# Kernel optimization log

Hardware: AMD Instinct MI355X
Metric: run time of the kernel (lower is better)

The kernel has to match this reference:

```python
import jax, jax.numpy as jnp
import numpy as np

D, DK, DV, H, DFF = 1024, 64, 64, 16, 4096
B, LD, LE = 8, 1024, 1024
NEG = -1e9


def _ln(x, g, b, eps=1e-5):
    m = jnp.mean(x, axis=-1, keepdims=True)
    v = jnp.var(x, axis=-1, keepdims=True)
    return (x - m) / jnp.sqrt(v + eps) * g + b


def _mha(q_src, kv_src, wq, bq, wk, bk, wv, bv, mask):
    # wq/wk: [H, D, DK], wv: [H, D, DV]; per-head linear projections (with bias)
    Q = jnp.einsum('bld,hdk->bhlk', q_src, wq) + bq[:, None, :]
    K = jnp.einsum('bld,hdk->bhlk', kv_src, wk) + bk[:, None, :]
    V = jnp.einsum('bld,hdv->bhlv', kv_src, wv) + bv[:, None, :]
    s = jnp.einsum('bhqk,bhmk->bhqm', Q, K) / jnp.sqrt(jnp.asarray(DK, Q.dtype))
    if mask is not None:
        s = s + mask
    a = jax.nn.softmax(s, axis=-1)
    o = jnp.einsum('bhqm,bhmv->bhqv', a, V)  # [B,H,L,DV]
    b_, h_, l_, dv_ = o.shape
    return jnp.transpose(o, (0, 2, 1, 3)).reshape(b_, l_, h_ * dv_)


def setup_inputs() -> dict:
    key = jax.random.key(0)
    ks = jax.random.split(key, 24)
    sc = 0.02
    inp = {
        'decoder_embedding': jax.random.normal(ks[0], (B, LD, D), jnp.float32),
        'encoder_output': jax.random.normal(ks[1], (B, LE, D), jnp.float32),
        # masked (self) attention heads, stacked over H
        'm_wq': jax.random.normal(ks[2], (H, D, DK)) * sc,
        'm_bq': jnp.zeros((H, DK)),
        'm_wk': jax.random.normal(ks[3], (H, D, DK)) * sc,
        'm_bk': jnp.zeros((H, DK)),
        'm_wv': jax.random.normal(ks[4], (H, D, DV)) * sc,
        'm_bv': jnp.zeros((H, DV)),
        # cross attention heads
        'c_wq': jax.random.normal(ks[5], (H, D, DK)) * sc,
        'c_bq': jnp.zeros((H, DK)),
        'c_wk': jax.random.normal(ks[6], (H, D, DK)) * sc,
        'c_bk': jnp.zeros((H, DK)),
        'c_wv': jax.random.normal(ks[7], (H, D, DV)) * sc,
        'c_bv': jnp.zeros((H, DV)),
        # FFN
        'ff_w1': jax.random.normal(ks[8], (D, DFF)) * sc,
        'ff_b1': jnp.zeros((DFF,)),
        'ff_w2': jax.random.normal(ks[9], (DFF, D)) * sc,
        'ff_b2': jnp.zeros((D,)),
        # LayerNorms (ln2 reused for the third norm, as in the source)
        'ln1_g': jnp.ones((D,)), 'ln1_b': jnp.zeros((D,)),
        'ln2_g': jnp.ones((D,)), 'ln2_b': jnp.zeros((D,)),
    }
    return inp


def reference(decoder_embedding, encoder_output,
              m_wq, m_bq, m_wk, m_bk, m_wv, m_bv,
              c_wq, c_bq, c_wk, c_bk, c_wv, c_bv,
              ff_w1, ff_b1, ff_w2, ff_b2,
              ln1_g, ln1_b, ln2_g, ln2_b):
    Ld = decoder_embedding.shape[1]
    causal = jnp.where(jnp.tril(jnp.ones((Ld, Ld), bool)), 0.0, NEG)[None, None]
    # masked self-attention + residual + LN1
    sa = _mha(decoder_embedding, decoder_embedding, m_wq, m_bq, m_wk, m_bk, m_wv, m_bv, causal)
    x = _ln(decoder_embedding + sa, ln1_g, ln1_b)
    # cross-attention (Q from decoder, K/V from encoder) + residual + LN2
    ca = _mha(x, encoder_output, c_wq, c_bq, c_wk, c_bk, c_wv, c_bv, None)
    x = _ln(x + ca, ln2_g, ln2_b)
    # FFN + residual + LN2 again (source reuses layer_norm2)
    ff = jnp.maximum(x @ ff_w1 + ff_b1, 0.0) @ ff_w2 + ff_b2
    return _ln(x + ff, ln2_g, ln2_b)
```

## Files before the change

kernel.cpp:

```cpp
#include <hip/hip_runtime.h>
#include <hip/hip_bf16.h>
#include <cstdint>

typedef __bf16 bf16x8 __attribute__((ext_vector_type(8)));
typedef float f32x4 __attribute__((ext_vector_type(4)));

union U128 { uint4 u; __bf16 h[8]; };
union U64  { uint2 u; __bf16 h[4]; };

#define DMODEL 1024
#define NHEAD  16
#define DHEAD  64

__device__ __forceinline__ void async_copy16(const void* g, void* l) {
  __builtin_amdgcn_global_load_lds(
      (const __attribute__((address_space(1))) void*)g,
      (__attribute__((address_space(3))) void*)l, 16, 0, 0);
}

__global__ __launch_bounds__(256) void k_cast(const float* __restrict__ s,
    __bf16* __restrict__ d, int n) {
  int i = (blockIdx.x * 256 + threadIdx.x) * 4;
  if (i < n) {
    float4 v = *(const float4*)(s + i);
    U64 o;
    o.h[0] = (__bf16)v.x; o.h[1] = (__bf16)v.y;
    o.h[2] = (__bf16)v.z; o.h[3] = (__bf16)v.w;
    *(uint2*)(d + i) = o.u;
  }
}

__global__ __launch_bounds__(256) void k_pack(float* __restrict__ dst,
    const float* __restrict__ s0, const float* __restrict__ s1,
    const float* __restrict__ s2, int n) {
  int i = blockIdx.x * 256 + threadIdx.x;
  if (i < n) dst[i] = s0[i];
  else if (i < 2 * n) dst[i] = s1[i - n];
  else if (i < 3 * n) dst[i] = s2[i - 2 * n];
}

__global__ __launch_bounds__(256) void k_transpose(const float* __restrict__ src,
    __bf16* __restrict__ dst, int R, int C) {
  __shared__ __bf16 tile[32][33];
  src += (size_t)blockIdx.z * R * C;
  dst += (size_t)blockIdx.z * R * C;
  int c0 = blockIdx.x * 32, r0 = blockIdx.y * 32;
  int tx = threadIdx.x & 31, ty = threadIdx.x >> 5;
  for (int i = ty; i < 32; i += 8)
    tile[i][tx] = (__bf16)src[(size_t)(r0 + i) * C + (c0 + tx)];
  __syncthreads();
  for (int i = ty; i < 32; i += 8)
    dst[(size_t)(c0 + i) * R + (r0 + tx)] = tile[tx][i];
}

template<bool RELU, typename OutT>
__global__ __launch_bounds__(256, 3) void k_gemm(const __bf16* __restrict__ A,
    const __bf16* __restrict__ Bt, const float* __restrict__ bias,
    OutT* __restrict__ C, int M, int N, int K) {
  __shared__ __bf16 As[128][64];
  __shared__ __bf16 Bs[128][64];
  const int m0 = blockIdx.y * 128, n0 = blockIdx.x * 128;
  const int t = threadIdx.x;
  const int wave = t >> 6, lane = t & 63;
  const int wm = (wave & 1) * 64, wn = (wave >> 1) * 64;
  const int lrow = lane & 15, quad = lane >> 4;
  const int r8 = lane >> 3;
  const int gG = (lane & 7) ^ (r8 & 7);
  const __bf16* Ap[4]; const __bf16* Bp[4];
  __bf16* lA[4]; __bf16* lB[4];
  for (int j = 0; j < 4; j++) {
    int rr = wave * 8 + j * 32 + r8;
    Ap[j] = A  + (size_t)(m0 + rr) * K + gG * 8;
    Bp[j] = Bt + (size_t)(n0 + rr) * K + gG * 8;
    lA[j] = &As[wave * 8 + j * 32][0];
    lB[j] = &Bs[wave * 8 + j * 32][0];
  }
  f32x4 acc[4][4] = {};
  for (int k0 = 0; k0 < K; k0 += 64) {
    __syncthreads();
    for (int j = 0; j < 4; j++) {
      async_copy16(Ap[j] + k0, lA[j]);
      async_copy16(Bp[j] + k0, lB[j]);
    }
    __syncthreads();
    for (int ks = 0; ks < 2; ks++) {
      bf16x8 af[4], bfv[4];
      for (int i = 0; i < 4; i++) {
        int ra = wm + i * 16 + lrow, rb = wn + i * 16 + lrow;
        af[i]  = *(const bf16x8*)&As[ra][(((ks * 4 + quad) ^ (ra & 7))) * 8];
        bfv[i] = *(const bf16x8*)&Bs[rb][(((ks * 4 + quad) ^ (rb & 7))) * 8];
      }
      for (int mi = 0; mi < 4; mi++)
        for (int ni = 0; ni < 4; ni++)
          acc[mi][ni] = __builtin_amdgcn_mfma_f32_16x16x32_bf16(af[mi], bfv[ni], acc[mi][ni], 0, 0, 0);
    }
  }
  for (int ni = 0; ni < 4; ni++) {
    int col = n0 + wn + ni * 16 + lrow;
    float bv = bias[col];
    for (int mi = 0; mi < 4; mi++) {
      int row = m0 + wm + mi * 16 + quad * 4;
      for (int r = 0; r < 4; r++) {
        float v = acc[mi][ni][r] + bv;
        if (RELU) v = fmaxf(v, 0.f);
        C[(size_t)(row + r) * N + col] = (OutT)v;
      }
    }
  }
}

template<bool CAUSAL>
__global__ __launch_bounds__(256, 4) void k_attn(const __bf16* __restrict__ Q,
    const __bf16* __restrict__ Kg, const __bf16* __restrict__ Vg,
    float* __restrict__ O, int Lq, int Lk, int qs, int kvs) {
  __shared__ alignas(16) __bf16 Qs[64][72];
  __shared__ alignas(16) __bf16 Ks[64][72];
  __shared__ alignas(16) __bf16 Vt[64][72];
  __shared__ alignas(16) __bf16 Ps[64][72];
  const int t = threadIdx.x;
  const int wave = t >> 6, lane = t & 63;
  const int lrow = lane & 15, quad = lane >> 4;
  const int wm16 = wave * 16;
  const int qt = CAUSAL ? (gridDim.x - 1 - blockIdx.x) : blockIdx.x;
  const int q0 = qt * 64;
  const int b = blockIdx.y >> 4, h = blockIdx.y & 15;
  const __bf16* Qb = Q  + (size_t)b * Lq * qs  + h * DHEAD;
  const __bf16* Kb = Kg + (size_t)b * Lk * kvs + h * DHEAD;
  const __bf16* Vb = Vg + (size_t)b * Lk * kvs + h * DHEAD;
  {
    int row = t >> 3, col = (t & 7) * 8;
    U128 u0, u1;
    u0.u = *(const uint4*)(Qb + (size_t)(q0 + row) * qs + col);
    u1.u = *(const uint4*)(Qb + (size_t)(q0 + row + 32) * qs + col);
    for (int j = 0; j < 8; j++) {
      u0.h[j] = (__bf16)((float)u0.h[j] * 0.125f);
      u1.h[j] = (__bf16)((float)u1.h[j] * 0.125f);
    }
    *(uint4*)&Qs[row][col]      = u0.u;
    *(uint4*)&Qs[row + 32][col] = u1.u;
  }
  f32x4 acc_o[4] = {};
  float m_r[4] = {-1e30f, -1e30f, -1e30f, -1e30f};
  float l_r[4] = {};
  const int nkt = CAUSAL ? (qt + 1) : (Lk / 64);
  const int krow = t >> 3, kcol = (t & 7) * 8;
  const int vkk = t & 63, vd8 = t >> 6;
  for (int kt = 0; kt < nkt; kt++) {
    const int k0 = kt * 64;
    uint4 ka  = *(const uint4*)(Kb + (size_t)(k0 + krow) * kvs + kcol);
    uint4 ka2 = *(const uint4*)(Kb + (size_t)(k0 + krow + 32) * kvs + kcol);
    uint4 va  = *(const uint4*)(Vb + (size_t)(k0 + vkk) * kvs + vd8 * 8);
    uint4 va2 = *(const uint4*)(Vb + (size_t)(k0 + vkk) * kvs + (vd8 + 4) * 8);
    __syncthreads();
    *(uint4*)&Ks[krow][kcol]      = ka;
    *(uint4*)&Ks[krow + 32][kcol] = ka2;
    { U128 u; u.u = va;  for (int j = 0; j < 8; j++) Vt[vd8 * 8 + j][vkk] = u.h[j]; }
    { U128 u; u.u = va2; for (int j = 0; j < 8; j++) Vt[(vd8 + 4) * 8 + j][vkk] = u.h[j]; }
    __syncthreads();
    f32x4 accs[4] = {};
    for (int ks = 0; ks < 2; ks++) {
      bf16x8 qa = *(const bf16x8*)&Qs[wm16 + lrow][ks * 32 + quad * 8];
      for (int nb = 0; nb < 4; nb++) {
        bf16x8 kfr = *(const bf16x8*)&Ks[nb * 16 + lrow][ks * 32 + quad * 8];
        accs[nb] = __builtin_amdgcn_mfma_f32_16x16x32_bf16(qa, kfr, accs[nb], 0, 0, 0);
      }
    }
    float pm[4] = {-1e30f, -1e30f, -1e30f, -1e30f};
    for (int nb = 0; nb < 4; nb++)
      for (int r = 0; r < 4; r++) {
        float s = accs[nb][r];
        if (CAUSAL && kt == qt)
          s = ((nb * 16 + lrow) <= (wm16 + quad * 4 + r)) ? s : -1e30f;
        accs[nb][r] = s;
        pm[r] = fmaxf(pm[r], s);
      }
    for (int msk = 1; msk <= 8; msk <<= 1)
      for (int r = 0; r < 4; r++)
        pm[r] = fmaxf(pm[r], __shfl_xor(pm[r], msk));
    float alpha[4], rs[4];
    for (int r = 0; r < 4; r++) {
      float mn = fmaxf(m_r[r], pm[r]);
      alpha[r] = __expf(m_r[r] - mn);
      m_r[r] = mn;
      float srow = 0.f;
      for (int nb = 0; nb < 4; nb++) {
        float p = __expf(accs[nb][r] - mn);
        accs[nb][r] = p;
        srow += p;
      }
      rs[r] = srow;
    }
    for (int msk = 1; msk <= 8; msk <<= 1)
      for (int r = 0; r < 4; r++)
        rs[r] += __shfl_xor(rs[r], msk);
    for (int r = 0; r < 4; r++)
      l_r[r] = l_r[r] * alpha[r] + rs[r];
    for (int ni = 0; ni < 4; ni++)
      for (int r = 0; r < 4; r++)
        acc_o[ni][r] *= alpha[r];
    for (int nb = 0; nb < 4; nb++)
      for (int r = 0; r < 4; r++)
        Ps[wm16 + quad * 4 + r][nb * 16 + lrow] = (__bf16)accs[nb][r];
    for (int ks = 0; ks < 2; ks++) {
      bf16x8 pa = *(const bf16x8*)&Ps[wm16 + lrow][ks * 32 + quad * 8];
      for (int ni = 0; ni < 4; ni++) {
        bf16x8 vfr = *(const bf16x8*)&Vt[ni * 16 + lrow][ks * 32 + quad * 8];
        acc_o[ni] = __builtin_amdgcn_mfma_f32_16x16x32_bf16(pa, vfr, acc_o[ni], 0, 0, 0);
      }
    }
  }
  float* Ob = O + (size_t)b * Lq * DMODEL + h * DHEAD;
  for (int r = 0; r < 4; r++) {
    float linv = 1.f / fmaxf(l_r[r], 1e-30f);
    int q = wm16 + quad * 4 + r;
    for (int ni = 0; ni < 4; ni++)
      Ob[(size_t)(q0 + q) * DMODEL + ni * 16 + lrow] = acc_o[ni][r] * linv;
  }
}

template<typename ResT, typename OutT>
__global__ __launch_bounds__(256) void k_ln_add(const ResT* __restrict__ a,
    const float* __restrict__ bres, const float* __restrict__ g,
    const float* __restrict__ be, OutT* __restrict__ out) {
  __shared__ float red[2][4];
  const int r = blockIdx.x, t = threadIdx.x;
  const size_t base = (size_t)r * DMODEL + t * 4;
  float x[4];
  for (int i = 0; i < 4; i++) x[i] = (float)a[base + i] + bres[base + i];
  float s  = x[0] + x[1] + x[2] + x[3];
  float s2 = x[0]*x[0] + x[1]*x[1] + x[2]*x[2] + x[3]*x[3];
  for (int off = 32; off > 0; off >>= 1) {
    s  += __shfl_down(s, off);
    s2 += __shfl_down(s2, off);
  }
  if ((t & 63) == 0) { red[0][t >> 6] = s; red[1][t >> 6] = s2; }
  __syncthreads();
  s  = red[0][0] + red[0][1] + red[0][2] + red[0][3];
  s2 = red[1][0] + red[1][1] + red[1][2] + red[1][3];
  const float mean = s * (1.f / DMODEL);
  const float var  = s2 * (1.f / DMODEL) - mean * mean;
  const float rstd = rsqrtf(var + 1e-5f);
  for (int i = 0; i < 4; i++)
    out[base + i] = (OutT)((x[i] - mean) * rstd * g[t * 4 + i] + be[t * 4 + i]);
}

extern "C" void kernel_launch(void* const* d_in, const int* in_sizes, int n_in,
                              void* d_out, int out_size, void* d_ws, size_t ws_size,
                              hipStream_t stream) {
  (void)in_sizes; (void)n_in; (void)out_size; (void)ws_size;
  const float* dec   = (const float*)d_in[0];
  const float* enc   = (const float*)d_in[1];
  const float* m_wq  = (const float*)d_in[2];
  const float* m_bq  = (const float*)d_in[3];
  const float* m_wk  = (const float*)d_in[4];
  const float* m_bk  = (const float*)d_in[5];
  const float* m_wv  = (const float*)d_in[6];
  const float* m_bv  = (const float*)d_in[7];
  const float* c_wq  = (const float*)d_in[8];
  const float* c_bq  = (const float*)d_in[9];
  const float* c_wk  = (const float*)d_in[10];
  const float* c_bk  = (const float*)d_in[11];
  const float* c_wv  = (const float*)d_in[12];
  const float* c_bv  = (const float*)d_in[13];
  const float* ff_w1 = (const float*)d_in[14];
  const float* ff_b1 = (const float*)d_in[15];
  const float* ff_w2 = (const float*)d_in[16];
  const float* ff_b2 = (const float*)d_in[17];
  const float* ln1_g = (const float*)d_in[18];
  const float* ln1_b = (const float*)d_in[19];
  const float* ln2_g = (const float*)d_in[20];
  const float* ln2_b = (const float*)d_in[21];

  char* w = (char*)d_ws;
  __bf16* decB = (__bf16*)(w);
  __bf16* encB = (__bf16*)(w + (16ull << 20));
  __bf16* X1b  = decB;
  __bf16* X2b  = encB;
  __bf16* WB   = (__bf16*)(w + (32ull << 20));
  float*  BP   = (float*) (w + (38ull << 20));
  __bf16* QKV  = (__bf16*)(w + (40ull << 20));
  __bf16* KV   = (__bf16*)(w + (40ull << 20));
  __bf16* Qc   = (__bf16*)(w + (72ull << 20));
  __bf16* FF   = (__bf16*)(w + (40ull << 20));
  float*  AO   = (float*) (w + (104ull << 20));
  float* out = (float*)d_out;

  const int M = 8192, NTOK = M * DMODEL;
  dim3 blk(256);
  dim3 gC(NTOK / 1024);
  dim3 gT6(2, 32, 16);
  dim3 gA(16, 128);
  dim3 gL(M);

  k_cast<<<gC, blk, 0, stream>>>(dec, decB, NTOK);
  k_cast<<<gC, blk, 0, stream>>>(enc, encB, NTOK);

  k_transpose<<<gT6, blk, 0, stream>>>(m_wq, WB, 1024, 64);
  k_transpose<<<gT6, blk, 0, stream>>>(m_wk, WB + (1 << 20), 1024, 64);
  k_transpose<<<gT6, blk, 0, stream>>>(m_wv, WB + (2 << 20), 1024, 64);
  k_pack<<<dim3(12), blk, 0, stream>>>(BP, m_bq, m_bk, m_bv, 1024);
  k_gemm<false, __bf16><<<dim3(24, 64), blk, 0, stream>>>(decB, WB, BP, QKV, M, 3072, 1024);
  k_attn<true><<<gA, blk, 0, stream>>>(QKV, QKV + 1024, QKV + 2048, AO, 1024, 1024, 3072, 3072);
  k_ln_add<float, __bf16><<<gL, blk, 0, stream>>>(dec, AO, ln1_g, ln1_b, X1b);

  k_transpose<<<gT6, blk, 0, stream>>>(c_wk, WB, 1024, 64);
  k_transpose<<<gT6, blk, 0, stream>>>(c_wv, WB + (1 << 20), 1024, 64);
  k_transpose<<<gT6, blk, 0, stream>>>(c_wq, WB + (2 << 20), 1024, 64);
  k_pack<<<dim3(8), blk, 0, stream>>>(BP, c_bk, c_bv, c_bv, 1024);
  k_gemm<false, __bf16><<<dim3(16, 64), blk, 0, stream>>>(encB, WB, BP, KV, M, 2048, 1024);
  k_gemm<false, __bf16><<<dim3(8, 64), blk, 0, stream>>>(X1b, WB + (2 << 20), c_bq, Qc, M, 1024, 1024);
  k_attn<false><<<gA, blk, 0, stream>>>(Qc, KV, KV + 1024, AO, 1024, 1024, 1024, 2048);
  k_ln_add<__bf16, __bf16><<<gL, blk, 0, stream>>>(X1b, AO, ln2_g, ln2_b, X2b);

  k_transpose<<<dim3(128, 32, 1), blk, 0, stream>>>(ff_w1, WB, 1024, 4096);
  k_gemm<true, __bf16><<<dim3(32, 64), blk, 0, stream>>>(X2b, WB, ff_b1, FF, M, 4096, 1024);
  k_transpose<<<dim3(32, 128, 1), blk, 0, stream>>>(ff_w2, WB, 4096, 1024);
  k_gemm<false, float><<<dim3(8, 64), blk, 0, stream>>>(FF, WB, ff_b2, AO, M, 1024, 4096);
  k_ln_add<__bf16, float><<<gL, blk, 0, stream>>>(X2b, AO, ln2_g, ln2_b, out);
}
```

Baseline: 804.3 us.

## Restructure attention kernel: transposed S, register-resident P, double-buffered K/V

```diff
diff --git a/kernel.cpp b/kernel.cpp
--- a/kernel.cpp
+++ b/kernel.cpp
@@ -3,14 +3,53 @@
 #include <cstdint>
 
 typedef __bf16 bf16x8 __attribute__((ext_vector_type(8)));
+typedef __bf16 bf16x4 __attribute__((ext_vector_type(4)));
+typedef short  short4v __attribute__((ext_vector_type(4)));
+typedef _Float16 f16x4 __attribute__((ext_vector_type(4)));
 typedef float f32x4 __attribute__((ext_vector_type(4)));
 
 union U128 { uint4 u; __bf16 h[8]; };
 union U64  { uint2 u; __bf16 h[4]; };
+union PV4  { uint2 u; bf16x4 b; short4v s; f16x4 f; };
 
 #define DMODEL 1024
 #define NHEAD  16
 #define DHEAD  64
+
+#if __has_builtin(__builtin_amdgcn_mfma_f32_16x16x16_bf16)
+#define PV_F16 0
+__device__ __forceinline__ f32x4 mfma16(PV4 a, PV4 b, f32x4 c) {
+  return __builtin_amdgcn_mfma_f32_16x16x16_bf16(a.b, b.b, c, 0, 0, 0);
+}
+#elif __has_builtin(__builtin_amdgcn_mfma_f32_16x16x16bf16_1k)
+#define PV_F16 0
+__device__ __forceinline__ f32x4 mfma16(PV4 a, PV4 b, f32x4 c) {
+  return __builtin_amdgcn_mfma_f32_16x16x16bf16_1k(a.s, b.s, c, 0, 0, 0);
+}
+#else
+#define PV_F16 1
+__device__ __forceinline__ f32x4 mfma16(PV4 a, PV4 b, f32x4 c) {
+  return __builtin_amdgcn_mfma_f32_16x16x16f16(a.f, b.f, c, 0, 0, 0);
+}
+#endif
+
+__device__ __forceinline__ uint16_t pv_bits(__bf16 v) {
+#if PV_F16
+  union { _Float16 f; uint16_t u; } x; x.f = (_Float16)(float)v; return x.u;
+#else
+  union { __bf16 b; uint16_t u; } x; x.b = v; return x.u;
+#endif
+}
+
+__device__ __forceinline__ PV4 pack4(float a, float b, float c, float d) {
+  PV4 r;
+#if PV_F16
+  r.f = (f16x4){(_Float16)a, (_Float16)b, (_Float16)c, (_Float16)d};
+#else
+  r.b = (bf16x4){(__bf16)a, (__bf16)b, (__bf16)c, (__bf16)d};
+#endif
+  return r;
+}
 
 __device__ __forceinline__ void async_copy16(const void* g, void* l) {
   __builtin_amdgcn_global_load_lds(
@@ -113,10 +152,8 @@
 __global__ __launch_bounds__(256, 4) void k_attn(const __bf16* __restrict__ Q,
     const __bf16* __restrict__ Kg, const __bf16* __restrict__ Vg,
     float* __restrict__ O, int Lq, int Lk, int qs, int kvs) {
-  __shared__ alignas(16) __bf16 Qs[64][72];
-  __shared__ alignas(16) __bf16 Ks[64][72];
-  __shared__ alignas(16) __bf16 Vt[64][72];
-  __shared__ alignas(16) __bf16 Ps[64][72];
+  __shared__ alignas(16) __bf16   Ks[2][64][72];
+  __shared__ alignas(16) uint16_t Vt[2][64][72];
   const int t = threadIdx.x;
   const int wave = t >> 6, lane = t & 63;
   const int lrow = lane & 15, quad = lane >> 4;
@@ -127,94 +164,84 @@
   const __bf16* Qb = Q  + (size_t)b * Lq * qs  + h * DHEAD;
   const __bf16* Kb = Kg + (size_t)b * Lk * kvs + h * DHEAD;
   const __bf16* Vb = Vg + (size_t)b * Lk * kvs + h * DHEAD;
-  {
-    int row = t >> 3, col = (t & 7) * 8;
-    U128 u0, u1;
-    u0.u = *(const uint4*)(Qb + (size_t)(q0 + row) * qs + col);
-    u1.u = *(const uint4*)(Qb + (size_t)(q0 + row + 32) * qs + col);
-    for (int j = 0; j < 8; j++) {
-      u0.h[j] = (__bf16)((float)u0.h[j] * 0.125f);
-      u1.h[j] = (__bf16)((float)u1.h[j] * 0.125f);
-    }
-    *(uint4*)&Qs[row][col]      = u0.u;
-    *(uint4*)&Qs[row + 32][col] = u1.u;
-  }
-  f32x4 acc_o[4] = {};
-  float m_r[4] = {-1e30f, -1e30f, -1e30f, -1e30f};
-  float l_r[4] = {};
+  bf16x8 qf[2];
+  for (int ks = 0; ks < 2; ks++) {
+    U128 u;
+    u.u = *(const uint4*)(Qb + (size_t)(q0 + wm16 + lrow) * qs + ks * 32 + quad * 8);
+    for (int j = 0; j < 8; j++) u.h[j] = (__bf16)((float)u.h[j] * 0.125f);
+    qf[ks] = *(const bf16x8*)u.h;
+  }
   const int nkt = CAUSAL ? (qt + 1) : (Lk / 64);
   const int krow = t >> 3, kcol = (t & 7) * 8;
-  const int vkk = t & 63, vd8 = t >> 6;
+  const int vkk = t & 63;
+  f32x4 acc_o[4] = {};
+  float m_r = -1e30f, l_r = 0.f;
+  uint4 ka, ka2, va, va2;
+  {
+    ka  = *(const uint4*)(Kb + (size_t)krow * kvs + kcol);
+    ka2 = *(const uint4*)(Kb + (size_t)(krow + 32) * kvs + kcol);
+    va  = *(const uint4*)(Vb + (size_t)vkk * kvs + wave * 8);
+    va2 = *(const uint4*)(Vb + (size_t)vkk * kvs + (wave + 4) * 8);
+  }
+  int c = 0;
   for (int kt = 0; kt < nkt; kt++) {
-    const int k0 = kt * 64;
-    uint4 ka  = *(const uint4*)(Kb + (size_t)(k0 + krow) * kvs + kcol);
-    uint4 ka2 = *(const uint4*)(Kb + (size_t)(k0 + krow + 32) * kvs + kcol);
-    uint4 va  = *(const uint4*)(Vb + (size_t)(k0 + vkk) * kvs + vd8 * 8);
-    uint4 va2 = *(const uint4*)(Vb + (size_t)(k0 + vkk) * kvs + (vd8 + 4) * 8);
+    const int kn = (kt + 1 < nkt) ? (kt + 1) * 64 : kt * 64;
+    uint4 na  = *(const uint4*)(Kb + (size_t)(kn + krow) * kvs + kcol);
+    uint4 na2 = *(const uint4*)(Kb + (size_t)(kn + krow + 32) * kvs + kcol);
+    uint4 nv  = *(const uint4*)(Vb + (size_t)(kn + vkk) * kvs + wave * 8);
+    uint4 nv2 = *(const uint4*)(Vb + (size_t)(kn + vkk) * kvs + (wave + 4) * 8);
+    *(uint4*)&Ks[c][krow][kcol]      = ka;
+    *(uint4*)&Ks[c][krow + 32][kcol] = ka2;
+    { U128 u; u.u = va;  for (int j = 0; j < 8; j++) Vt[c][wave * 8 + j][vkk] = pv_bits(u.h[j]); }
+    { U128 u; u.u = va2; for (int j = 0; j < 8; j++) Vt[c][(wave + 4) * 8 + j][vkk] = pv_bits(u.h[j]); }
     __syncthreads();
-    *(uint4*)&Ks[krow][kcol]      = ka;
-    *(uint4*)&Ks[krow + 32][kcol] = ka2;
-    { U128 u; u.u = va;  for (int j = 0; j < 8; j++) Vt[vd8 * 8 + j][vkk] = u.h[j]; }
-    { U128 u; u.u = va2; for (int j = 0; j < 8; j++) Vt[(vd8 + 4) * 8 + j][vkk] = u.h[j]; }
-    __syncthreads();
-    f32x4 accs[4] = {};
-    for (int ks = 0; ks < 2; ks++) {
-      bf16x8 qa = *(const bf16x8*)&Qs[wm16 + lrow][ks * 32 + quad * 8];
+    f32x4 st[4] = {};
+    for (int ks = 0; ks < 2; ks++)
       for (int nb = 0; nb < 4; nb++) {
-        bf16x8 kfr = *(const bf16x8*)&Ks[nb * 16 + lrow][ks * 32 + quad * 8];
-        accs[nb] = __builtin_amdgcn_mfma_f32_16x16x32_bf16(qa, kfr, accs[nb], 0, 0, 0);
-      }
-    }
-    float pm[4] = {-1e30f, -1e30f, -1e30f, -1e30f};
+        bf16x8 kf = *(const bf16x8*)&Ks[c][nb * 16 + lrow][ks * 32 + quad * 8];
+        st[nb] = __builtin_amdgcn_mfma_f32_16x16x32_bf16(kf, qf[ks], st[nb], 0, 0, 0);
+      }
+    float pm = -1e30f;
     for (int nb = 0; nb < 4; nb++)
       for (int r = 0; r < 4; r++) {
-        float s = accs[nb][r];
+        float s = st[nb][r];
         if (CAUSAL && kt == qt)
-          s = ((nb * 16 + lrow) <= (wm16 + quad * 4 + r)) ? s : -1e30f;
-        accs[nb][r] = s;
-        pm[r] = fmaxf(pm[r], s);
-      }
-    for (int msk = 1; msk <= 8; msk <<= 1)
-      for (int r = 0; r < 4; r++)
-        pm[r] = fmaxf(pm[r], __shfl_xor(pm[r], msk));
-    float alpha[4], rs[4];
-    for (int r = 0; r < 4; r++) {
-      float mn = fmaxf(m_r[r], pm[r]);
-      alpha[r] = __expf(m_r[r] - mn);
-      m_r[r] = mn;
-      float srow = 0.f;
-      for (int nb = 0; nb < 4; nb++) {
-        float p = __expf(accs[nb][r] - mn);
-        accs[nb][r] = p;
-        srow += p;
-      }
-      rs[r] = srow;
+          if (nb * 16 + quad * 4 + r > wm16 + lrow) s = -1e30f;
+        st[nb][r] = s;
+        pm = fmaxf(pm, s);
+      }
+    pm = fmaxf(pm, __shfl_xor(pm, 16));
+    pm = fmaxf(pm, __shfl_xor(pm, 32));
+    float mn = fmaxf(m_r, pm);
+    float alpha = __expf(m_r - mn);
+    m_r = mn;
+    float rs = 0.f;
+    PV4 pf[4];
+    for (int nb = 0; nb < 4; nb++) {
+      float p0 = __expf(st[nb][0] - mn), p1 = __expf(st[nb][1] - mn);
+      float p2 = __expf(st[nb][2] - mn), p3 = __expf(st[nb][3] - mn);
+      rs += (p0 + p1) + (p2 + p3);
+      pf[nb] = pack4(p0, p1, p2, p3);
     }
-    for (int msk = 1; msk <= 8; msk <<= 1)
-      for (int r = 0; r < 4; r++)
-        rs[r] += __shfl_xor(rs[r], msk);
-    for (int r = 0; r < 4; r++)
-      l_r[r] = l_r[r] * alpha[r] + rs[r];
+    rs += __shfl_xor(rs, 16);
+    rs += __shfl_xor(rs, 32);
+    l_r = l_r * alpha + rs;
     for (int ni = 0; ni < 4; ni++)
-      for (int r = 0; r < 4; r++)
-        acc_o[ni][r] *= alpha[r];
+      for (int r = 0; r < 4; r++) acc_o[ni][r] *= alpha;
     for (int nb = 0; nb < 4; nb++)
-      for (int r = 0; r < 4; r++)
-        Ps[wm16 + quad * 4 + r][nb * 16 + lrow] = (__bf16)accs[nb][r];
-    for (int ks = 0; ks < 2; ks++) {
-      bf16x8 pa = *(const bf16x8*)&Ps[wm16 + lrow][ks * 32 + quad * 8];
       for (int ni = 0; ni < 4; ni++) {
-        bf16x8 vfr = *(const bf16x8*)&Vt[ni * 16 + lrow][ks * 32 + quad * 8];
-        acc_o[ni] = __builtin_amdgcn_mfma_f32_16x16x32_bf16(pa, vfr, acc_o[ni], 0, 0, 0);
-      }
-    }
-  }
-  float* Ob = O + (size_t)b * Lq * DMODEL + h * DHEAD;
-  for (int r = 0; r < 4; r++) {
-    float linv = 1.f / fmaxf(l_r[r], 1e-30f);
-    int q = wm16 + quad * 4 + r;
-    for (int ni = 0; ni < 4; ni++)
-      Ob[(size_t)(q0 + q) * DMODEL + ni * 16 + lrow] = acc_o[ni][r] * linv;
+        PV4 vf; vf.u = *(const uint2*)&Vt[c][ni * 16 + lrow][nb * 16 + quad * 4];
+        acc_o[ni] = mfma16(vf, pf[nb], acc_o[ni]);
+      }
+    ka = na; ka2 = na2; va = nv; va2 = nv2;
+    c ^= 1;
+  }
+  const float linv = 1.f / fmaxf(l_r, 1e-30f);
+  float* orow = O + (size_t)b * Lq * DMODEL + (size_t)(q0 + wm16 + lrow) * DMODEL + h * DHEAD;
+  for (int ni = 0; ni < 4; ni++) {
+    float4 v = { acc_o[ni][0] * linv, acc_o[ni][1] * linv,
+                 acc_o[ni][2] * linv, acc_o[ni][3] * linv };
+    *(float4*)(orow + ni * 16 + quad * 4) = v;
   }
 }
 
```

Result: faster. 719.3 us (-10.6%).
